# Kernel tuning notes

Hardware: AMD Instinct MI355X
Metric: run time of the kernel (lower is better)

## Reference

```python
import jax, jax.numpy as jnp
import numpy as np

EPS = 1e-5
SCALES = jnp.array([7.0, 7.0, 4.0], dtype=jnp.float32)  # (W, H, T) per source buffer
OUT_T, OUT_H, OUT_W = 3, 5, 5


def _roi_align3d(feat, start, end):
    """feat: [C,T,H,W]; start/end: [3] = (x, y, t). One sample per bin (bin center),
    trilinear interpolation, out-of-bounds -> 0 (standard ROIAlign convention)."""
    C, T, H, W = feat.shape
    dt = feat.dtype

    def centers(s, e, n):
        b = (e - s) / n
        return s + (jnp.arange(n, dtype=dt) + 0.5) * b

    xc = centers(start[0], end[0], OUT_W)  # [Wo]
    yc = centers(start[1], end[1], OUT_H)  # [Ho]
    tc = centers(start[2], end[2], OUT_T)  # [To]

    def prep(c, size):
        valid = ((c >= -1.0) & (c <= size)).astype(dt)
        c = jnp.clip(c, 0.0, size - 1)
        lo = jnp.floor(c).astype(jnp.int32)
        hi = jnp.minimum(lo + 1, size - 1)
        f = c - lo.astype(dt)
        return (lo, hi), ((1.0 - f) * valid, f * valid)

    ti, tw = prep(tc, T)
    yi, yw = prep(yc, H)
    xi, xw = prep(xc, W)

    out = jnp.zeros((C, OUT_T, OUT_H, OUT_W), dtype=dt)
    for a in range(2):
        for b in range(2):
            for c in range(2):
                g = feat[:, ti[a][:, None, None], yi[b][None, :, None], xi[c][None, None, :]]
                w = tw[a][:, None, None] * yw[b][None, :, None] * xw[c][None, None, :]
                out = out + g * w
    return out


def setup_inputs() -> dict:
    key = jax.random.key(0)
    k0, k1, k2 = jax.random.split(key, 3)
    B, C, T, H, W = 128, 1024, 4, 7, 7
    R = 256
    x = jax.random.normal(k0, (B, C, T, H, W), jnp.float32)
    w1 = jax.random.normal(k1, (R, C), jnp.float32) / np.sqrt(C).astype(np.float32)
    w2 = jax.random.normal(k2, (6, R), jnp.float32) / np.sqrt(R).astype(np.float32)
    return dict(
        x=x, w1=w1,
        g1=jnp.ones((R,), jnp.float32), b1=jnp.zeros((R,), jnp.float32),
        m1=jnp.zeros((R,), jnp.float32), v1=jnp.ones((R,), jnp.float32),
        w2=w2,
        g2=jnp.ones((6,), jnp.float32), b2=jnp.zeros((6,), jnp.float32),
        m2=jnp.zeros((6,), jnp.float32), v2=jnp.ones((6,), jnp.float32),
    )


def reference(x, w1, g1, b1, m1, v1, w2, g2, b2, m2, v2):
    # roi head: conv1x1x1 -> BN(eval) -> HSwish -> global avgpool -> conv1x1x1 -> BN(eval)
    h = jnp.einsum('bcthw,rc->brthw', x, w1)
    s1 = (g1 / jnp.sqrt(v1 + EPS))
    h = (h - m1[None, :, None, None, None]) * s1[None, :, None, None, None] + b1[None, :, None, None, None]
    h = h * jnp.clip(h + 3.0, 0.0, 6.0) * (1.0 / 6.0)  # HSwish
    h = h.mean(axis=(2, 3, 4))                          # AvgPool3d over full (T,H,W) -> [B,R]
    logits = h @ w2.T
    logits = (logits - m2) * (g2 / jnp.sqrt(v2 + EPS)) + b2  # [B,6]
    raw = jax.nn.sigmoid(logits)
    roi_start = 0.5 * raw[:, :3] * SCALES              # (x1,y1,t1)
    roi_end = (1.0 - 0.5 * raw[:, 3:]) * SCALES        # (x2,y2,t2)
    return jax.vmap(_roi_align3d)(x, roi_start, roi_end)  # [B,C,3,5,5]
```

## Files before the change

kernel.cpp:

```cpp
#include <hip/hip_runtime.h>

typedef __bf16 bf16x8 __attribute__((ext_vector_type(8)));
typedef float f32x4 __attribute__((ext_vector_type(4)));

#define EPS_F 1e-5f

__device__ __forceinline__ unsigned short f2bf(float f) {
    unsigned int u;
    __builtin_memcpy(&u, &f, 4);
    unsigned int r = (u + 0x7fffu + ((u >> 16) & 1u)) >> 16;
    return (unsigned short)r;
}

__global__ __launch_bounds__(512) void k_gemm_pool(
    const float* __restrict__ x,
    const float* __restrict__ w1,
    const float* __restrict__ g1,
    const float* __restrict__ b1,
    const float* __restrict__ m1,
    const float* __restrict__ v1,
    float* __restrict__ pooled)
{
    constexpr int LDK = 40;
    __shared__ unsigned short Alds[224 * LDK];
    __shared__ unsigned short Blds[64 * LDK];
    __shared__ float pool_lds[2][64];

    const int b   = blockIdx.x;
    const int r0  = blockIdx.y * 64;
    const int tid = threadIdx.x;
    const int wave = tid >> 6, lane = tid & 63;
    const int wm = wave >> 2, wn = wave & 3;
    const int q  = lane >> 4, ln = lane & 15;

    f32x4 acc[7];
#pragma unroll
    for (int i = 0; i < 7; i++) acc[i] = (f32x4){0.f, 0.f, 0.f, 0.f};

    const int c4  = tid & 7;
    const int p4  = tid >> 3;
    const bool a_act = (p4 < 56);
    const bool a_val = (p4 < 49);
    const float* xb = x + (size_t)b * 1024 * 196 + p4 * 4;

    const int rB = tid >> 3, k16 = tid & 7;

    for (int kc = 0; kc < 1024; kc += 32) {
        __syncthreads();
        {
            const float4 f = *(const float4*)(w1 + (size_t)(r0 + rB) * 1024 + kc + k16 * 4);
            ushort4 o;
            o.x = f2bf(f.x); o.y = f2bf(f.y); o.z = f2bf(f.z); o.w = f2bf(f.w);
            *(ushort4*)&Blds[rB * LDK + k16 * 4] = o;
        }
        if (a_act) {
            float fv[4][4];
            if (a_val) {
#pragma unroll
                for (int i = 0; i < 4; i++) {
                    const float4 f = *(const float4*)(xb + (size_t)(kc + c4 * 4 + i) * 196);
                    fv[i][0] = f.x; fv[i][1] = f.y; fv[i][2] = f.z; fv[i][3] = f.w;
                }
            } else {
#pragma unroll
                for (int i = 0; i < 4; i++)
#pragma unroll
                    for (int j = 0; j < 4; j++) fv[i][j] = 0.f;
            }
#pragma unroll
            for (int j = 0; j < 4; j++) {
                ushort4 o;
                o.x = f2bf(fv[0][j]);
                o.y = f2bf(fv[1][j]);
                o.z = f2bf(fv[2][j]);
                o.w = f2bf(fv[3][j]);
                *(ushort4*)&Alds[(p4 * 4 + j) * LDK + c4 * 4] = o;
            }
        }
        __syncthreads();
        const bf16x8 bfr = *(const bf16x8*)&Blds[(wn * 16 + ln) * LDK + q * 8];
#pragma unroll
        for (int mi = 0; mi < 7; mi++) {
            const int mt = wm * 7 + mi;
            const bf16x8 af = *(const bf16x8*)&Alds[(mt * 16 + ln) * LDK + q * 8];
            acc[mi] = __builtin_amdgcn_mfma_f32_16x16x32_bf16(af, bfr, acc[mi], 0, 0, 0);
        }
    }

    float psum = 0.f;
    {
        const int r = r0 + wn * 16 + ln;
        const float s1 = g1[r] * rsqrtf(v1[r] + EPS_F);
        const float mu = m1[r];
        const float be = b1[r];
#pragma unroll
        for (int mi = 0; mi < 7; mi++) {
            const int mt = wm * 7 + mi;
#pragma unroll
            for (int i = 0; i < 4; i++) {
                const int m = mt * 16 + q * 4 + i;
                if (m < 196) {
                    float v = acc[mi][i];
                    v = (v - mu) * s1 + be;
                    const float g = fminf(fmaxf(v + 3.f, 0.f), 6.f);
                    psum += v * g * (1.f / 6.f);
                }
            }
        }
    }
    psum += __shfl_xor(psum, 16, 64);
    psum += __shfl_xor(psum, 32, 64);
    if (lane < 16) pool_lds[wm][wn * 16 + lane] = psum;
    __syncthreads();
    if (tid < 64)
        pooled[b * 256 + r0 + tid] =
            (pool_lds[0][tid] + pool_lds[1][tid]) * (1.f / 196.f);
}

__global__ __launch_bounds__(64) void k_logits(
    const float* __restrict__ pooled,
    const float* __restrict__ w2,
    const float* __restrict__ g2,
    const float* __restrict__ b2,
    const float* __restrict__ m2,
    const float* __restrict__ v2,
    float* __restrict__ roi)
{
    const int b = blockIdx.x, t = threadIdx.x;
    const float4 p4 = ((const float4*)(pooled + b * 256))[t];
    float part[6];
#pragma unroll
    for (int j = 0; j < 6; j++) {
        const float4 w = *(const float4*)(w2 + j * 256 + t * 4);
        part[j] = p4.x * w.x + p4.y * w.y + p4.z * w.z + p4.w * w.w;
    }
#pragma unroll
    for (int j = 0; j < 6; j++)
#pragma unroll
        for (int off = 32; off >= 1; off >>= 1)
            part[j] += __shfl_xor(part[j], off, 64);
    if (t == 0) {
        const float SC[3] = {7.f, 7.f, 4.f};
        float raw[6];
#pragma unroll
        for (int j = 0; j < 6; j++) {
            float l = part[j];
            const float s = g2[j] * rsqrtf(v2[j] + EPS_F);
            l = (l - m2[j]) * s + b2[j];
            raw[j] = 1.f / (1.f + expf(-l));
        }
#pragma unroll
        for (int d = 0; d < 3; d++) {
            roi[b * 6 + d]     = 0.5f * raw[d] * SC[d];
            roi[b * 6 + 3 + d] = (1.f - 0.5f * raw[3 + d]) * SC[d];
        }
    }
}

__device__ __forceinline__ void prep1(float s, float e, int n, int size, int i,
                                      int& lo, int& hi, float& w0, float& w1)
{
    const float bsz = (e - s) / (float)n;
    float c = s + ((float)i + 0.5f) * bsz;
    const float valid = (c >= -1.f && c <= (float)size) ? 1.f : 0.f;
    c = fminf(fmaxf(c, 0.f), (float)(size - 1));
    lo = (int)floorf(c);
    hi = min(lo + 1, size - 1);
    const float f = c - (float)lo;
    w0 = (1.f - f) * valid;
    w1 = f * valid;
}

__global__ __launch_bounds__(256) void k_roi(
    const float* __restrict__ x,
    const float* __restrict__ roi,
    float* __restrict__ out)
{
    __shared__ float xs[32 * 200];
    __shared__ int   soff[8][80];
    __shared__ float swt[8][80];

    const int b = blockIdx.x, c0 = blockIdx.y * 32;
    const int tid = threadIdx.x;

    const float* xb = x + ((size_t)b * 1024 + c0) * 196;
#pragma unroll
    for (int k = 0; k < 7; k++) {
        const int i4 = tid + k * 256;
        if (i4 < 1568) {
            const int c = i4 / 49, pq = i4 % 49;
            const float4 v = *(const float4*)(xb + c * 196 + pq * 4);
            *(float4*)&xs[c * 200 + pq * 4] = v;
        }
    }
    if (tid < 75) {
        const int po = tid;
        const int to = po / 25, rem = po % 25, yo = rem / 5, xo = rem % 5;
        const float sx = roi[b * 6 + 0], ex = roi[b * 6 + 3];
        const float sy = roi[b * 6 + 1], ey = roi[b * 6 + 4];
        const float st = roi[b * 6 + 2], et = roi[b * 6 + 5];
        int tl, th, yl, yh, xl, xh;
        float tw0, tw1, yw0, yw1, xw0, xw1;
        prep1(st, et, 3, 4, to, tl, th, tw0, tw1);
        prep1(sy, ey, 5, 7, yo, yl, yh, yw0, yw1);
        prep1(sx, ex, 5, 7, xo, xl, xh, xw0, xw1);
#pragma unroll
        for (int s = 0; s < 8; s++) {
            const int   ti = (s & 4) ? th : tl;
            const int   yi = (s & 2) ? yh : yl;
            const int   xi = (s & 1) ? xh : xl;
            const float w = ((s & 4) ? tw1 : tw0) *
                            ((s & 2) ? yw1 : yw0) *
                            ((s & 1) ? xw1 : xw0);
            soff[s][po] = ti * 49 + yi * 7 + xi;
            swt[s][po]  = w;
        }
    }
    __syncthreads();

    const size_t obase = ((size_t)b * 1024 + c0) * 75;
#pragma unroll
    for (int k = 0; k < 10; k++) {
        const int e = tid + k * 256;
        if (e < 2400) {
            const int c = e / 75, po = e % 75;
            const float* row = &xs[c * 200];
            float v = 0.f;
#pragma unroll
            for (int s = 0; s < 8; s++)
                v += swt[s][po] * row[soff[s][po]];
            out[obase + e] = v;
        }
    }
}

extern "C" void kernel_launch(void* const* d_in, const int* in_sizes, int n_in,
                              void* d_out, int out_size, void* d_ws, size_t ws_size,
                              hipStream_t stream)
{
    const float* x  = (const float*)d_in[0];
    const float* w1 = (const float*)d_in[1];
    const float* g1 = (const float*)d_in[2];
    const float* b1 = (const float*)d_in[3];
    const float* m1 = (const float*)d_in[4];
    const float* v1 = (const float*)d_in[5];
    const float* w2 = (const float*)d_in[6];
    const float* g2 = (const float*)d_in[7];
    const float* b2 = (const float*)d_in[8];
    const float* m2 = (const float*)d_in[9];
    const float* v2 = (const float*)d_in[10];

    float* pooled = (float*)d_ws;
    float* roi    = pooled + 128 * 256;
    float* out    = (float*)d_out;

    k_gemm_pool<<<dim3(128, 4), 512, 0, stream>>>(x, w1, g1, b1, m1, v1, pooled);
    k_logits<<<128, 64, 0, stream>>>(pooled, w2, g2, b2, m2, v2, roi);
    k_roi<<<dim3(128, 32), 256, 0, stream>>>(x, roi, out);
}
```

Baseline: 239.3 us.

## Split GEMM over spatial chunks, pre-convert w1, fuse logits into ROI kernel

The 1x1x1 conv GEMM is repartitioned: each block now covers all 256 output channels for a 49-position spatial chunk, instead of 64 channels across all 196 positions. This stops x from being re-read four times, at the cost of writing four partial pooled sums. w1 is converted to bf16 once in a separate kernel, and the logits/sigmoid step is fused into the ROI kernel, which reduces the partials and computes the ROI box per block. The ROI kernel now keeps per-output offsets and weights in registers, so each thread handles 8 channels. The trade-offs are redundant logits computation in every block and scalar, strided A loads with 2-byte LDS stores.

Measured after the change: 252.7 us. +5.6%, slower.

```diff
diff --git a/kernel.cpp b/kernel.cpp
--- a/kernel.cpp
+++ b/kernel.cpp
@@ -5,156 +5,122 @@
 
 #define EPS_F 1e-5f
 
-__device__ __forceinline__ unsigned short f2bf(float f) {
-    unsigned int u;
-    __builtin_memcpy(&u, &f, 4);
-    unsigned int r = (u + 0x7fffu + ((u >> 16) & 1u)) >> 16;
-    return (unsigned short)r;
+__device__ __forceinline__ unsigned short cvtbf(float f) {
+    __bf16 h = (__bf16)f;
+    unsigned short u;
+    __builtin_memcpy(&u, &h, 2);
+    return u;
+}
+
+__global__ __launch_bounds__(256) void k_cvt_w1(
+    const float* __restrict__ w1, unsigned short* __restrict__ w1b)
+{
+    const int idx = (blockIdx.x * 256 + threadIdx.x) * 8;
+    const float4 f0 = *(const float4*)(w1 + idx);
+    const float4 f1 = *(const float4*)(w1 + idx + 4);
+    ushort4 o0, o1;
+    o0.x = cvtbf(f0.x); o0.y = cvtbf(f0.y); o0.z = cvtbf(f0.z); o0.w = cvtbf(f0.w);
+    o1.x = cvtbf(f1.x); o1.y = cvtbf(f1.y); o1.z = cvtbf(f1.z); o1.w = cvtbf(f1.w);
+    *(ushort4*)(w1b + idx)     = o0;
+    *(ushort4*)(w1b + idx + 4) = o1;
 }
 
 __global__ __launch_bounds__(512) void k_gemm_pool(
     const float* __restrict__ x,
-    const float* __restrict__ w1,
+    const unsigned short* __restrict__ w1b,
     const float* __restrict__ g1,
     const float* __restrict__ b1,
     const float* __restrict__ m1,
     const float* __restrict__ v1,
-    float* __restrict__ pooled)
-{
-    constexpr int LDK = 40;
-    __shared__ unsigned short Alds[224 * LDK];
-    __shared__ unsigned short Blds[64 * LDK];
-    __shared__ float pool_lds[2][64];
+    float* __restrict__ pooled_part)
+{
+    constexpr int LDK = 36;
+    __shared__ unsigned short Alds[64 * LDK];
+    __shared__ unsigned short Blds[256 * LDK];
+    __shared__ float pool_sc[2][256];
 
     const int b   = blockIdx.x;
-    const int r0  = blockIdx.y * 64;
+    const int pc  = blockIdx.y;
+    const int p0  = pc * 49;
     const int tid = threadIdx.x;
     const int wave = tid >> 6, lane = tid & 63;
     const int wm = wave >> 2, wn = wave & 3;
     const int q  = lane >> 4, ln = lane & 15;
 
-    f32x4 acc[7];
-#pragma unroll
-    for (int i = 0; i < 7; i++) acc[i] = (f32x4){0.f, 0.f, 0.f, 0.f};
-
-    const int c4  = tid & 7;
-    const int p4  = tid >> 3;
-    const bool a_act = (p4 < 56);
-    const bool a_val = (p4 < 49);
-    const float* xb = x + (size_t)b * 1024 * 196 + p4 * 4;
-
-    const int rB = tid >> 3, k16 = tid & 7;
+    f32x4 acc[2][4];
+#pragma unroll
+    for (int i = 0; i < 2; i++)
+#pragma unroll
+        for (int j = 0; j < 4; j++) acc[i][j] = (f32x4){0.f, 0.f, 0.f, 0.f};
+
+    const int cl = tid >> 4, psub = tid & 15;
+    const float* xa = x + ((size_t)b * 1024 + cl) * 196 + p0 + psub;
+    const int rb = tid >> 1, kh = (tid & 1) * 16;
+    const unsigned short* wrow = w1b + rb * 1024 + kh;
 
     for (int kc = 0; kc < 1024; kc += 32) {
         __syncthreads();
         {
-            const float4 f = *(const float4*)(w1 + (size_t)(r0 + rB) * 1024 + kc + k16 * 4);
-            ushort4 o;
-            o.x = f2bf(f.x); o.y = f2bf(f.y); o.z = f2bf(f.z); o.w = f2bf(f.w);
-            *(ushort4*)&Blds[rB * LDK + k16 * 4] = o;
-        }
-        if (a_act) {
-            float fv[4][4];
-            if (a_val) {
-#pragma unroll
-                for (int i = 0; i < 4; i++) {
-                    const float4 f = *(const float4*)(xb + (size_t)(kc + c4 * 4 + i) * 196);
-                    fv[i][0] = f.x; fv[i][1] = f.y; fv[i][2] = f.z; fv[i][3] = f.w;
-                }
-            } else {
-#pragma unroll
-                for (int i = 0; i < 4; i++)
-#pragma unroll
-                    for (int j = 0; j < 4; j++) fv[i][j] = 0.f;
+            const uint4 v0 = *(const uint4*)(wrow + kc);
+            const uint4 v1 = *(const uint4*)(wrow + kc + 8);
+            *(uint4*)&Blds[rb * LDK + kh]     = v0;
+            *(uint4*)&Blds[rb * LDK + kh + 8] = v1;
+        }
+        {
+            const float* xi = xa + (size_t)kc * 196;
+#pragma unroll
+            for (int j = 0; j < 4; j++) {
+                const int p = psub + j * 16;
+                if (p < 49)
+                    Alds[p * LDK + cl] = cvtbf(xi[j * 16]);
             }
-#pragma unroll
-            for (int j = 0; j < 4; j++) {
-                ushort4 o;
-                o.x = f2bf(fv[0][j]);
-                o.y = f2bf(fv[1][j]);
-                o.z = f2bf(fv[2][j]);
-                o.w = f2bf(fv[3][j]);
-                *(ushort4*)&Alds[(p4 * 4 + j) * LDK + c4 * 4] = o;
-            }
         }
         __syncthreads();
-        const bf16x8 bfr = *(const bf16x8*)&Blds[(wn * 16 + ln) * LDK + q * 8];
-#pragma unroll
-        for (int mi = 0; mi < 7; mi++) {
-            const int mt = wm * 7 + mi;
-            const bf16x8 af = *(const bf16x8*)&Alds[(mt * 16 + ln) * LDK + q * 8];
-            acc[mi] = __builtin_amdgcn_mfma_f32_16x16x32_bf16(af, bfr, acc[mi], 0, 0, 0);
-        }
-    }
-
-    float psum = 0.f;
-    {
-        const int r = r0 + wn * 16 + ln;
+        bf16x8 bfr[4], afr[2];
+#pragma unroll
+        for (int ni = 0; ni < 4; ni++)
+            bfr[ni] = *(const bf16x8*)&Blds[(wn * 64 + ni * 16 + ln) * LDK + q * 8];
+#pragma unroll
+        for (int mi = 0; mi < 2; mi++)
+            afr[mi] = *(const bf16x8*)&Alds[(wm * 32 + mi * 16 + ln) * LDK + q * 8];
+#pragma unroll
+        for (int mi = 0; mi < 2; mi++)
+#pragma unroll
+            for (int ni = 0; ni < 4; ni++)
+                acc[mi][ni] = __builtin_amdgcn_mfma_f32_16x16x32_bf16(
+                    afr[mi], bfr[ni], acc[mi][ni], 0, 0, 0);
+    }
+
+    float psum[4] = {0.f, 0.f, 0.f, 0.f};
+#pragma unroll
+    for (int ni = 0; ni < 4; ni++) {
+        const int r = wn * 64 + ni * 16 + ln;
         const float s1 = g1[r] * rsqrtf(v1[r] + EPS_F);
         const float mu = m1[r];
         const float be = b1[r];
 #pragma unroll
-        for (int mi = 0; mi < 7; mi++) {
-            const int mt = wm * 7 + mi;
+        for (int mi = 0; mi < 2; mi++)
 #pragma unroll
             for (int i = 0; i < 4; i++) {
-                const int m = mt * 16 + q * 4 + i;
-                if (m < 196) {
-                    float v = acc[mi][i];
+                const int pl = wm * 32 + mi * 16 + q * 4 + i;
+                if (pl < 49) {
+                    float v = acc[mi][ni][i];
                     v = (v - mu) * s1 + be;
                     const float g = fminf(fmaxf(v + 3.f, 0.f), 6.f);
-                    psum += v * g * (1.f / 6.f);
+                    psum[ni] += v * g * (1.f / 6.f);
                 }
             }
-        }
-    }
-    psum += __shfl_xor(psum, 16, 64);
-    psum += __shfl_xor(psum, 32, 64);
-    if (lane < 16) pool_lds[wm][wn * 16 + lane] = psum;
+    }
+#pragma unroll
+    for (int ni = 0; ni < 4; ni++) {
+        psum[ni] += __shfl_xor(psum[ni], 16, 64);
+        psum[ni] += __shfl_xor(psum[ni], 32, 64);
+        if (lane < 16) pool_sc[wm][wn * 64 + ni * 16 + lane] = psum[ni];
+    }
     __syncthreads();
-    if (tid < 64)
-        pooled[b * 256 + r0 + tid] =
-            (pool_lds[0][tid] + pool_lds[1][tid]) * (1.f / 196.f);
-}
-
-__global__ __launch_bounds__(64) void k_logits(
-    const float* __restrict__ pooled,
-    const float* __restrict__ w2,
-    const float* __restrict__ g2,
-    const float* __restrict__ b2,
-    const float* __restrict__ m2,
-    const float* __restrict__ v2,
-    float* __restrict__ roi)
-{
-    const int b = blockIdx.x, t = threadIdx.x;
-    const float4 p4 = ((const float4*)(pooled + b * 256))[t];
-    float part[6];
-#pragma unroll
-    for (int j = 0; j < 6; j++) {
-        const float4 w = *(const float4*)(w2 + j * 256 + t * 4);
-        part[j] = p4.x * w.x + p4.y * w.y + p4.z * w.z + p4.w * w.w;
-    }
-#pragma unroll
-    for (int j = 0; j < 6; j++)
-#pragma unroll
-        for (int off = 32; off >= 1; off >>= 1)
-            part[j] += __shfl_xor(part[j], off, 64);
-    if (t == 0) {
-        const float SC[3] = {7.f, 7.f, 4.f};
-        float raw[6];
-#pragma unroll
-        for (int j = 0; j < 6; j++) {
-            float l = part[j];
-            const float s = g2[j] * rsqrtf(v2[j] + EPS_F);
-            l = (l - m2[j]) * s + b2[j];
-            raw[j] = 1.f / (1.f + expf(-l));
-        }
-#pragma unroll
-        for (int d = 0; d < 3; d++) {
-            roi[b * 6 + d]     = 0.5f * raw[d] * SC[d];
-            roi[b * 6 + 3 + d] = (1.f - 0.5f * raw[3 + d]) * SC[d];
-        }
-    }
+    if (tid < 256)
+        pooled_part[((size_t)pc * 128 + b) * 256 + tid] =
+            pool_sc[0][tid] + pool_sc[1][tid];
 }
 
 __device__ __forceinline__ void prep1(float s, float e, int n, int size, int i,
@@ -171,65 +137,99 @@
     w1 = f * valid;
 }
 
-__global__ __launch_bounds__(256) void k_roi(
+__global__ __launch_bounds__(320) void k_roi(
     const float* __restrict__ x,
-    const float* __restrict__ roi,
+    const float* __restrict__ pooled_part,
+    const float* __restrict__ w2,
+    const float* __restrict__ g2,
+    const float* __restrict__ b2,
+    const float* __restrict__ m2,
+    const float* __restrict__ v2,
     float* __restrict__ out)
 {
     __shared__ float xs[32 * 200];
-    __shared__ int   soff[8][80];
-    __shared__ float swt[8][80];
+    __shared__ float red[6][4];
+    __shared__ float roi_s[6];
 
     const int b = blockIdx.x, c0 = blockIdx.y * 32;
     const int tid = threadIdx.x;
+    const int wave = tid >> 6, lane = tid & 63;
 
     const float* xb = x + ((size_t)b * 1024 + c0) * 196;
 #pragma unroll
-    for (int k = 0; k < 7; k++) {
-        const int i4 = tid + k * 256;
+    for (int k = 0; k < 5; k++) {
+        const int i4 = tid + k * 320;
         if (i4 < 1568) {
-            const int c = i4 / 49, pq = i4 % 49;
+            const int c = i4 / 49, pq = i4 - c * 49;
             const float4 v = *(const float4*)(xb + c * 196 + pq * 4);
             *(float4*)&xs[c * 200 + pq * 4] = v;
         }
     }
-    if (tid < 75) {
-        const int po = tid;
+    float part[6] = {0.f, 0.f, 0.f, 0.f, 0.f, 0.f};
+    if (tid < 256) {
+        const size_t o = (size_t)b * 256 + tid;
+        const float pv = (pooled_part[o] + pooled_part[32768 + o] +
+                          pooled_part[65536 + o] + pooled_part[98304 + o]) *
+                         (1.f / 196.f);
+#pragma unroll
+        for (int j = 0; j < 6; j++) part[j] = pv * w2[j * 256 + tid];
+    }
+#pragma unroll
+    for (int j = 0; j < 6; j++)
+#pragma unroll
+        for (int off = 32; off >= 1; off >>= 1)
+            part[j] += __shfl_xor(part[j], off, 64);
+    if (lane == 0 && wave < 4)
+#pragma unroll
+        for (int j = 0; j < 6; j++) red[j][wave] = part[j];
+    __syncthreads();
+    if (tid == 0) {
+        const float SC[3] = {7.f, 7.f, 4.f};
+#pragma unroll
+        for (int j = 0; j < 6; j++) {
+            float l = red[j][0] + red[j][1] + red[j][2] + red[j][3];
+            const float s = g2[j] * rsqrtf(v2[j] + EPS_F);
+            l = (l - m2[j]) * s + b2[j];
+            const float raw = 1.f / (1.f + expf(-l));
+            const int d = (j < 3) ? j : j - 3;
+            roi_s[j] = (j < 3) ? 0.5f * raw * SC[d]
+                               : (1.f - 0.5f * raw) * SC[d];
+        }
+    }
+    __syncthreads();
+
+    const int po = tid % 80;
+    const int cg = tid / 80;
+    int   offr[8];
+    float wtr[8];
+    if (po < 75) {
         const int to = po / 25, rem = po % 25, yo = rem / 5, xo = rem % 5;
-        const float sx = roi[b * 6 + 0], ex = roi[b * 6 + 3];
-        const float sy = roi[b * 6 + 1], ey = roi[b * 6 + 4];
-        const float st = roi[b * 6 + 2], et = roi[b * 6 + 5];
         int tl, th, yl, yh, xl, xh;
         float tw0, tw1, yw0, yw1, xw0, xw1;
-        prep1(st, et, 3, 4, to, tl, th, tw0, tw1);
-        prep1(sy, ey, 5, 7, yo, yl, yh, yw0, yw1);
-        prep1(sx, ex, 5, 7, xo, xl, xh, xw0, xw1);
+        prep1(roi_s[2], roi_s[5], 3, 4, to, tl, th, tw0, tw1);
+        prep1(roi_s[1], roi_s[4], 5, 7, yo, yl, yh, yw0, yw1);
+        prep1(roi_s[0], roi_s[3], 5, 7, xo, xl, xh, xw0, xw1);
 #pragma unroll
         for (int s = 0; s < 8; s++) {
             const int   ti = (s & 4) ? th : tl;
             const int   yi = (s & 2) ? yh : yl;
             const int   xi = (s & 1) ? xh : xl;
-            const float w = ((s & 4) ? tw1 : tw0) *
-                            ((s & 2) ? yw1 : yw0) *
-                            ((s & 1) ? xw1 : xw0);
-            soff[s][po] = ti * 49 + yi * 7 + xi;
-            swt[s][po]  = w;
-        }
-    }
-    __syncthreads();
-
-    const size_t obase = ((size_t)b * 1024 + c0) * 75;
-#pragma unroll
-    for (int k = 0; k < 10; k++) {
-        const int e = tid + k * 256;
-        if (e < 2400) {
-            const int c = e / 75, po = e % 75;
-            const float* row = &xs[c * 200];
+            offr[s] = ti * 49 + yi * 7 + xi;
+            wtr[s]  = ((s & 4) ? tw1 : tw0) *
+                      ((s & 2) ? yw1 : yw0) *
+                      ((s & 1) ? xw1 : xw0);
+        }
+    }
+    if (po < 75) {
+        const size_t obase = ((size_t)b * 1024 + c0 + cg * 8) * 75 + po;
+#pragma unroll
+        for (int k = 0; k < 8; k++) {
+            const float* row = &xs[(cg * 8 + k) * 200];
             float v = 0.f;
 #pragma unroll
             for (int s = 0; s < 8; s++)
-                v += swt[s][po] * row[soff[s][po]];
-            out[obase + e] = v;
+                v += wtr[s] * row[offr[s]];
+            out[obase + (size_t)k * 75] = v;
         }
     }
 }
@@ -250,11 +250,11 @@
     const float* m2 = (const float*)d_in[9];
     const float* v2 = (const float*)d_in[10];
 
-    float* pooled = (float*)d_ws;
-    float* roi    = pooled + 128 * 256;
-    float* out    = (float*)d_out;
-
-    k_gemm_pool<<<dim3(128, 4), 512, 0, stream>>>(x, w1, g1, b1, m1, v1, pooled);
-    k_logits<<<128, 64, 0, stream>>>(pooled, w2, g2, b2, m2, v2, roi);
-    k_roi<<<dim3(128, 32), 256, 0, stream>>>(x, roi, out);
-}
+    unsigned short* w1b   = (unsigned short*)d_ws;
+    float* pooled_part    = (float*)((char*)d_ws + 524288);
+    float* out            = (float*)d_out;
+
+    k_cvt_w1<<<128, 256, 0, stream>>>(w1, w1b);
+    k_gemm_pool<<<dim3(128, 4), 512, 0, stream>>>(x, w1b, g1, b1, m1, v1, pooled_part);
+    k_roi<<<dim3(128, 32), 320, 0, stream>>>(x, pooled_part, w2, g2, b2, m2, v2, out);
+}
```
